# Kernel tuning notes

Hardware: AMD Instinct MI355X
Metric: run time of the kernel (lower is better)

Reference implementation:

```python
import jax, jax.numpy as jnp
import numpy as np

CAPACITY = 65536
HIDDEN = 512
NUM_HASHES = 8
HASH_SIZE = 16
BATCH = 2048


def setup_inputs() -> dict:
    key = jax.random.key(0)
    ks = jax.random.split(key, 6)
    scale = 1.0 / np.sqrt(HIDDEN)
    query = jax.random.normal(ks[0], (BATCH, HIDDEN), dtype=jnp.float32)
    memory_keys = jax.random.normal(ks[1], (CAPACITY, HIDDEN), dtype=jnp.float32) * scale
    memory_values = jax.random.normal(ks[2], (CAPACITY, HIDDEN), dtype=jnp.float32) * scale
    hash_projections = jax.random.normal(ks[3], (NUM_HASHES, HIDDEN, HASH_SIZE), dtype=jnp.float32) * scale
    out_w = jax.random.normal(ks[4], (HIDDEN, HIDDEN), dtype=jnp.float32) * scale  # torch Linear weight [out,in]
    out_b = jnp.zeros((HIDDEN,), dtype=jnp.float32)
    return {"query": query, "memory_keys": memory_keys, "memory_values": memory_values,
            "hash_projections": hash_projections, "out_w": out_w, "out_b": out_b, "top_k": 32}


def _compute_hash(x, hash_projections):
    # x: [m, h] -> hash bits [m, num_hashes] in {0,1}
    # einsum 'bh,nhd->bnd' then sum over d then sign-threshold
    proj = jnp.einsum('mh,nhd->mnd', x, hash_projections)
    return (proj.sum(-1) > 0).astype(jnp.int32)


def reference(query, memory_keys, memory_values, hash_projections, out_w, out_b, top_k):
    b, h = query.shape
    q_hash = _compute_hash(query, hash_projections)                    # [b, n]
    k_hash = _compute_hash(memory_keys, hash_projections)              # [c, n] (no_grad in torch)
    # Hamming distance via +/-1 dot product: dot = n - 2*dist (avoids [b,c,n] bool tensor)
    qf = (q_hash * 2 - 1).astype(jnp.float32)
    kf = (k_hash * 2 - 1).astype(jnp.float32)
    dot = jnp.einsum('bn,cn->bc', qf, kf)                              # [b, c]
    hash_dist = ((NUM_HASHES - dot) * 0.5).astype(jnp.int32)           # [b, c]
    k = min(top_k, memory_keys.shape[0])
    _, top_indices = jax.lax.top_k(-hash_dist, k)                      # smallest distances, [b, k]
    selected_keys = memory_keys[top_indices]                           # [b, k, h]
    selected_values = memory_values[top_indices]                       # [b, k, h]
    scores = jnp.einsum('bh,bkh->bk', query, selected_keys) / np.sqrt(h).astype(np.float32)
    attn = jax.nn.softmax(scores, axis=-1)
    memory_output = jnp.einsum('bk,bkh->bh', attn, selected_values)    # [b, h]
    return memory_output @ out_w.T + out_b
```

## Files before the change

kernel.cpp:

```cpp
#include <hip/hip_runtime.h>
#include <stdint.h>

#define BATCH  2048
#define HID    512
#define CAP    65536
#define NHASH  8
#define TOPK   32
#define NSLICE 16
#define SLICE_SZ (CAP / NSLICE)
#define ROWS_TILE 16

typedef unsigned int   u32;
typedef unsigned long long u64;
typedef double d4 __attribute__((ext_vector_type(4)));

__global__ __launch_bounds__(256) void k_psum(const float* __restrict__ proj,
                                              double* __restrict__ psumT) {
    int h = blockIdx.x * blockDim.x + threadIdx.x;
    if (h >= HID) return;
    for (int n = 0; n < NHASH; n++) {
        const float* p = proj + ((size_t)n * HID + h) * 16;
        double s = 0.0;
        #pragma unroll
        for (int d = 0; d < 16; d++) s += (double)p[d];
        psumT[(size_t)h * NHASH + n] = s;
    }
}

__global__ __launch_bounds__(256, 3) void k_hash(const float* __restrict__ x, int rows,
                                                 const double* __restrict__ psumT,
                                                 unsigned char* __restrict__ outb,
                                                 u32* __restrict__ hist16, int do_hist) {
    __shared__ __align__(16) float sX[ROWS_TILE * HID];
    __shared__ double sAcc4[4][ROWS_TILE][8];

    const int tid  = threadIdx.x;
    const int w    = tid >> 6;
    const int m    = (tid & 63) & 15;
    const int kk   = (tid & 63) >> 4;

    d4 z = {0.0, 0.0, 0.0, 0.0};
    d4 pr = __builtin_amdgcn_mfma_f64_16x16x4f64((double)(m + 1), 1.0, z, 0, 0, 0);
    d4 pc = __builtin_amdgcn_mfma_f64_16x16x4f64(1.0, (double)(m + 1), z, 0, 0, 0);
    d4 pp = __builtin_amdgcn_mfma_f64_16x16x4f64((double)(1 << kk),
                                                 (double)(1 << (4 * kk)), z, 0, 0, 0);
    int rowOf[4], colOf[4];
    #pragma unroll
    for (int i = 0; i < 4; i++) {
        rowOf[i] = (int)(pr[i] * 0.25) - 1;
        colOf[i] = (int)(pc[i] * 0.25) - 1;
    }
    u32 pb = (u32)pp[0];
    u32 pairPacked = 0;
    #pragma unroll
    for (int e = 0; e < 16; e++)
        if ((pb >> e) & 1u) pairPacked |= (u32)(e & 3) << (2 * (e >> 2));

    const int kAdj = (int)((pairPacked >> (2 * kk)) & 3u);
    double bfrag[32];
    #pragma unroll
    for (int j = 0; j < 32; j++) {
        int kp = 128 * w + 4 * j + kAdj;
        bfrag[j] = (m < 8) ? psumT[(size_t)kp * NHASH + m] : 0.0;
    }

    const int sw = (m & 7) << 2;
    const int nTiles = rows / ROWS_TILE;

    for (int t = blockIdx.x; t < nTiles; t += gridDim.x) {
        const int rowBase = t * ROWS_TILE;

        for (int i = tid; i < ROWS_TILE * 128; i += 256) {
            int r = i >> 7, G = i & 127;
            float4 v = ((const float4*)(x + (size_t)(rowBase + r) * HID))[G];
            ((float4*)sX)[r * 128 + (G ^ (r & 7))] = v;
        }
        __syncthreads();

        d4 acc = {0.0, 0.0, 0.0, 0.0};
        const float* sxm = sX + m * HID;
        #pragma unroll
        for (int j = 0; j < 32; j++) {
            int k = 128 * w + 4 * j + kk;
            double a = (double)sxm[k ^ sw];
            acc = __builtin_amdgcn_mfma_f64_16x16x4f64(a, bfrag[j], acc, 0, 0, 0);
        }
        #pragma unroll
        for (int i = 0; i < 4; i++) {
            if (((unsigned)rowOf[i] < (unsigned)ROWS_TILE) && ((unsigned)colOf[i] < 8u))
                sAcc4[w][rowOf[i]][colOf[i]] = acc[i];
        }
        __syncthreads();

        if (tid < ROWS_TILE) {
            u32 byte = 0;
            #pragma unroll
            for (int n = 0; n < 8; n++) {
                double s = sAcc4[0][tid][n] + sAcc4[1][tid][n]
                         + sAcc4[2][tid][n] + sAcc4[3][tid][n];
                if (s > 0.0) byte |= (1u << n);
            }
            outb[rowBase + tid] = (unsigned char)byte;
            if (do_hist) atomicAdd(&hist16[((rowBase + tid) / SLICE_SZ) * 256 + byte], 1u);
        }
    }
}

__global__ __launch_bounds__(256) void k_scan(const u32* __restrict__ hist16,
                                              u32* __restrict__ bucketCnt,
                                              u32* __restrict__ bucketOff,
                                              u32* __restrict__ off16) {
    __shared__ u32 sh[256], sh2[256];
    int v = threadIdx.x;
    u32 tot = 0;
    for (int s = 0; s < NSLICE; s++) tot += hist16[s * 256 + v];
    bucketCnt[v] = tot;
    sh[v] = tot;
    __syncthreads();
    if (v == 0) {
        u32 run = 0;
        for (int u = 0; u < 256; u++) { sh2[u] = run; run += sh[u]; }
    }
    __syncthreads();
    u32 base = sh2[v];
    bucketOff[v] = base;
    for (int s = 0; s < NSLICE; s++) { off16[s * 256 + v] = base; base += hist16[s * 256 + v]; }
}

__global__ __launch_bounds__(256) void k_compact(const unsigned char* __restrict__ khash,
                                                 const u32* __restrict__ off16,
                                                 u32* __restrict__ bucketList) {
    __shared__ unsigned char sh[SLICE_SZ];
    int s  = blockIdx.x & (NSLICE - 1);
    int bg = blockIdx.x >> 4;
    ((uint4*)sh)[threadIdx.x] = ((const uint4*)(khash + (size_t)s * SLICE_SZ))[threadIdx.x];
    __syncthreads();
    int w = threadIdx.x >> 6, lane = threadIdx.x & 63;
    int v = bg * 4 + w;
    u32 base = off16[s * 256 + v];
    for (int i = 0; i < SLICE_SZ / 64; i++) {
        int c = i * 64 + lane;
        unsigned char byte = sh[c];
        bool hit = (byte == (unsigned char)v);
        u64 m = __ballot(hit);
        if (hit) {
            int rank = __popcll(m & ((1ull << lane) - 1ull));
            bucketList[base + rank] = (u32)(s * SLICE_SZ + c);
        }
        base += (u32)__popcll(m);
    }
}

__global__ __launch_bounds__(256) void k_select(const unsigned char* __restrict__ qhash,
                                                const u32* __restrict__ bucketCnt,
                                                const u32* __restrict__ bucketOff,
                                                const u32* __restrict__ bucketList,
                                                int* __restrict__ topIdx) {
    __shared__ u32 sCnt[256], sOff[256];
    __shared__ int sPos[4];
    int tid = threadIdx.x;
    sCnt[tid] = bucketCnt[tid];
    sOff[tid] = bucketOff[tid];
    int w = tid >> 6, lane = tid & 63;
    if (lane == 0) sPos[w] = 0;
    __syncthreads();

    int q = blockIdx.x * 4 + w;
    u32 qh = qhash[q];

    int d[4]; u32 cnt[4], off[4];
    #pragma unroll
    for (int jj = 0; jj < 4; jj++) {
        int v = lane + jj * 64;
        d[jj] = __popc(qh ^ (u32)v);
        cnt[jj] = sCnt[v];
        off[jj] = sOff[v];
    }

    u32 ct[9];
    #pragma unroll
    for (int t = 0; t < 9; t++) {
        u32 c = 0;
        #pragma unroll
        for (int jj = 0; jj < 4; jj++) c += (d[jj] == t) ? cnt[jj] : 0u;
        #pragma unroll
        for (int s = 32; s >= 1; s >>= 1) c += __shfl_xor(c, s, 64);
        ct[t] = c;
    }

    int dcut = 0; u32 run = 0, before = 0;
    for (int t = 0; t < 9; t++) {
        before = run; run += ct[t];
        if (run >= TOPK) { dcut = t; break; }
    }
    int need = TOPK - (int)before;

    #pragma unroll
    for (int jj = 0; jj < 4; jj++) {
        if (d[jj] < dcut && cnt[jj] > 0) {
            int base = atomicAdd(&sPos[w], (int)cnt[jj]);
            for (u32 e = 0; e < cnt[jj]; e++)
                topIdx[q * TOPK + base + e] = (int)bucketList[off[jj] + e];
        }
    }

    int nb = 0;
    #pragma unroll
    for (int jj = 0; jj < 4; jj++) nb += (d[jj] == dcut) ? 1 : 0;
    #pragma unroll
    for (int s = 32; s >= 1; s >>= 1) nb += __shfl_xor(nb, s, 64);

    if (nb == 1) {
        u32 boff = 0xFFFFFFFFu;
        #pragma unroll
        for (int jj = 0; jj < 4; jj++) if (d[jj] == dcut) boff = off[jj];
        #pragma unroll
        for (int s = 32; s >= 1; s >>= 1) boff = min(boff, __shfl_xor(boff, s, 64));
        if (lane < need)
            topIdx[q * TOPK + (int)before + lane] = (int)bucketList[boff + lane];
    } else {
        u32 pos[4], end[4]; int val[4];
        #pragma unroll
        for (int jj = 0; jj < 4; jj++) {
            if (d[jj] == dcut && cnt[jj] > 0) {
                pos[jj] = off[jj]; end[jj] = off[jj] + cnt[jj];
                val[jj] = (int)bucketList[pos[jj]];
            } else { pos[jj] = 0; end[jj] = 0; val[jj] = 0x7fffffff; }
        }
        for (int it = 0; it < need; it++) {
            int m = min(min(val[0], val[1]), min(val[2], val[3]));
            int g = m;
            #pragma unroll
            for (int s = 32; s >= 1; s >>= 1) g = min(g, __shfl_xor(g, s, 64));
            if (lane == 0) topIdx[q * TOPK + (int)before + it] = g;
            if (m == g && g != 0x7fffffff) {
                #pragma unroll
                for (int jj = 0; jj < 4; jj++) {
                    if (val[jj] == g) {
                        pos[jj]++;
                        val[jj] = (pos[jj] < end[jj]) ? (int)bucketList[pos[jj]] : 0x7fffffff;
                        break;
                    }
                }
            }
        }
    }
}

__global__ __launch_bounds__(256) void k_attn(const float* __restrict__ keys,
                                              const float* __restrict__ vals,
                                              const float* __restrict__ query,
                                              const int* __restrict__ topIdx,
                                              float* __restrict__ mo) {
    __shared__ int sIdx[TOPK];
    __shared__ float sSc[TOPK], sE[TOPK];
    int b = blockIdx.x, tid = threadIdx.x;
    if (tid < TOPK) sIdx[tid] = topIdx[b * TOPK + tid];
    __syncthreads();

    int w = tid >> 6, lane = tid & 63;
    const float4* qp = (const float4*)(query + (size_t)b * HID + lane * 8);
    float4 qa = qp[0], qb = qp[1];

    for (int i = w * 8; i < w * 8 + 8; i++) {
        int idx = sIdx[i];
        const float4* kp = (const float4*)(keys + (size_t)idx * HID + lane * 8);
        float4 ka = kp[0], kb = kp[1];
        float dot = qa.x * ka.x + qa.y * ka.y + qa.z * ka.z + qa.w * ka.w
                  + qb.x * kb.x + qb.y * kb.y + qb.z * kb.z + qb.w * kb.w;
        #pragma unroll
        for (int s = 32; s >= 1; s >>= 1) dot += __shfl_xor(dot, s, 64);
        if (lane == 0) sSc[i] = dot * 0.04419417382415922f;
    }
    __syncthreads();

    if (tid < TOPK) {
        float m = -1e30f;
        for (int i = 0; i < TOPK; i++) m = fmaxf(m, sSc[i]);
        sE[tid] = expf(sSc[tid] - m);
    }
    __syncthreads();

    float sum = 0.f;
    for (int i = 0; i < TOPK; i++) sum += sE[i];
    float inv = 1.0f / sum;

    int h0 = tid, h1 = tid + 256;
    float a0 = 0.f, a1 = 0.f;
    for (int i = 0; i < TOPK; i++) {
        int idx = sIdx[i];
        float e = sE[i];
        a0 += e * vals[(size_t)idx * HID + h0];
        a1 += e * vals[(size_t)idx * HID + h1];
    }
    mo[(size_t)b * HID + h0] = a0 * inv;
    mo[(size_t)b * HID + h1] = a1 * inv;
}

__global__ __launch_bounds__(256) void k_transpose(const float* __restrict__ w,
                                                   float* __restrict__ wt) {
    __shared__ float tile[64][65];
    int bx = blockIdx.x, by = blockIdx.y;
    int tx = threadIdx.x & 63, ty = threadIdx.x >> 6;
    for (int r = ty; r < 64; r += 4)
        tile[r][tx] = w[(size_t)(by * 64 + r) * HID + bx * 64 + tx];
    __syncthreads();
    for (int r = ty; r < 64; r += 4)
        wt[(size_t)(bx * 64 + r) * HID + by * 64 + tx] = tile[tx][r];
}

__global__ __launch_bounds__(256) void k_proj(const float* __restrict__ mo,
                                              const float* __restrict__ wt,
                                              const float* __restrict__ bias,
                                              float* __restrict__ out) {
    int tid = threadIdx.x;
    int o = (blockIdx.x & 1) * 256 + tid;
    int bb = (blockIdx.x >> 1) * 8;
    float acc[8];
    #pragma unroll
    for (int r = 0; r < 8; r++) acc[r] = 0.f;
    for (int h = 0; h < HID; h++) {
        float wv = wt[(size_t)h * HID + o];
        #pragma unroll
        for (int r = 0; r < 8; r++)
            acc[r] += mo[(size_t)(bb + r) * HID + h] * wv;
    }
    float bv = bias[o];
    #pragma unroll
    for (int r = 0; r < 8; r++)
        out[(size_t)(bb + r) * HID + o] = acc[r] + bv;
}

extern "C" void kernel_launch(void* const* d_in, const int* in_sizes, int n_in,
                              void* d_out, int out_size, void* d_ws, size_t ws_size,
                              hipStream_t stream) {
    const float* query = (const float*)d_in[0];
    const float* keys  = (const float*)d_in[1];
    const float* vals  = (const float*)d_in[2];
    const float* proj  = (const float*)d_in[3];
    const float* outw  = (const float*)d_in[4];
    const float* outb  = (const float*)d_in[5];
    float* out = (float*)d_out;

    char* ws = (char*)d_ws;
    double*        psumT      = (double*)(ws + 0);
    unsigned char* qhash      = (unsigned char*)(ws + 32768);
    unsigned char* khash      = (unsigned char*)(ws + 34816);
    u32*           hist16     = (u32*)(ws + 100352);
    u32*           bucketCnt  = (u32*)(ws + 116736);
    u32*           bucketOff  = (u32*)(ws + 117760);
    u32*           off16      = (u32*)(ws + 118784);
    u32*           bucketList = (u32*)(ws + 135168);
    int*           topIdx     = (int*)(ws + 397312);
    float*         mo         = (float*)(ws + 659456);
    float*         wt         = (float*)(ws + 4853760);
    (void)in_sizes; (void)n_in; (void)out_size; (void)ws_size;

    hipMemsetAsync(hist16, 0, 16384, stream);
    k_psum<<<2, 256, 0, stream>>>(proj, psumT);
    k_hash<<<128, 256, 0, stream>>>(query, BATCH, psumT, qhash, hist16, 0);
    k_hash<<<1024, 256, 0, stream>>>(keys, CAP, psumT, khash, hist16, 1);
    k_scan<<<1, 256, 0, stream>>>(hist16, bucketCnt, bucketOff, off16);
    k_compact<<<1024, 256, 0, stream>>>(khash, off16, bucketList);
    k_select<<<BATCH / 4, 256, 0, stream>>>(qhash, bucketCnt, bucketOff, bucketList, topIdx);
    k_attn<<<BATCH, 256, 0, stream>>>(keys, vals, query, topIdx, mo);
    k_transpose<<<dim3(8, 8), 256, 0, stream>>>(outw, wt);
    k_proj<<<512, 256, 0, stream>>>(mo, wt, outb, out);
}
```

Measured before the change: 384.4 us.

## Fuse launches: merge prep kernels, query/key hashing, and selection into attention

Merges the memset, psum and weight transpose into one prep kernel, and runs query and key hashing in a single launch. Top-k selection now happens inside the attention kernel, where wave 0 writes the indices straight to shared memory, so the topIdx buffer and its round trip go away. The scan uses a wave-shuffle prefix instead of a serial loop, and the value accumulation uses float2 loads. The aim is to cut launch count and serial overhead. The cost is that the other waves in each attention block sit idle while wave 0 does the selection.

```diff
diff --git a/kernel.cpp b/kernel.cpp
--- a/kernel.cpp
+++ b/kernel.cpp
@@ -9,28 +9,50 @@
 #define NSLICE 16
 #define SLICE_SZ (CAP / NSLICE)
 #define ROWS_TILE 16
+#define QTILES (BATCH / ROWS_TILE)
+#define KTILES (CAP / ROWS_TILE)
+#define QGRID  128
+#define KGRID  1024
 
 typedef unsigned int   u32;
 typedef unsigned long long u64;
 typedef double d4 __attribute__((ext_vector_type(4)));
 
-__global__ __launch_bounds__(256) void k_psum(const float* __restrict__ proj,
-                                              double* __restrict__ psumT) {
-    int h = blockIdx.x * blockDim.x + threadIdx.x;
-    if (h >= HID) return;
-    for (int n = 0; n < NHASH; n++) {
-        const float* p = proj + ((size_t)n * HID + h) * 16;
-        double s = 0.0;
-        #pragma unroll
-        for (int d = 0; d < 16; d++) s += (double)p[d];
-        psumT[(size_t)h * NHASH + n] = s;
-    }
-}
-
-__global__ __launch_bounds__(256, 3) void k_hash(const float* __restrict__ x, int rows,
+__global__ __launch_bounds__(256) void k_prep(const float* __restrict__ proj,
+                                              double* __restrict__ psumT,
+                                              u32* __restrict__ hist16,
+                                              const float* __restrict__ w,
+                                              float* __restrict__ wt) {
+    __shared__ float tile[64][65];
+    int bi = blockIdx.x, tid = threadIdx.x;
+    if (bi < 2) {
+        int g = bi * 256 + tid;
+        for (int i = g; i < NSLICE * 256; i += 512) hist16[i] = 0;
+        int h = g;
+        for (int n = 0; n < NHASH; n++) {
+            const float* p = proj + ((size_t)n * HID + h) * 16;
+            double s = 0.0;
+            #pragma unroll
+            for (int d = 0; d < 16; d++) s += (double)p[d];
+            psumT[(size_t)h * NHASH + n] = s;
+        }
+    } else {
+        int b = bi - 2, bx = b & 7, by = b >> 3;
+        int tx = tid & 63, ty = tid >> 6;
+        for (int r = ty; r < 64; r += 4)
+            tile[r][tx] = w[(size_t)(by * 64 + r) * HID + bx * 64 + tx];
+        __syncthreads();
+        for (int r = ty; r < 64; r += 4)
+            wt[(size_t)(bx * 64 + r) * HID + by * 64 + tx] = tile[tx][r];
+    }
+}
+
+__global__ __launch_bounds__(256, 3) void k_hash(const float* __restrict__ query,
+                                                 const float* __restrict__ keys,
                                                  const double* __restrict__ psumT,
-                                                 unsigned char* __restrict__ outb,
-                                                 u32* __restrict__ hist16, int do_hist) {
+                                                 unsigned char* __restrict__ qhash,
+                                                 unsigned char* __restrict__ khash,
+                                                 u32* __restrict__ hist16) {
     __shared__ __align__(16) float sX[ROWS_TILE * HID];
     __shared__ double sAcc4[4][ROWS_TILE][8];
 
@@ -38,6 +60,14 @@
     const int w    = tid >> 6;
     const int m    = (tid & 63) & 15;
     const int kk   = (tid & 63) >> 4;
+
+    const int isQ = (blockIdx.x < QGRID);
+    const float* x        = isQ ? query : keys;
+    unsigned char* outb   = isQ ? qhash : khash;
+    const int nTiles      = isQ ? QTILES : KTILES;
+    const int b0          = isQ ? blockIdx.x : (blockIdx.x - QGRID);
+    const int gstride     = isQ ? QGRID : KGRID;
+    const int do_hist     = !isQ;
 
     d4 z = {0.0, 0.0, 0.0, 0.0};
     d4 pr = __builtin_amdgcn_mfma_f64_16x16x4f64((double)(m + 1), 1.0, z, 0, 0, 0);
@@ -65,9 +95,8 @@
     }
 
     const int sw = (m & 7) << 2;
-    const int nTiles = rows / ROWS_TILE;
-
-    for (int t = blockIdx.x; t < nTiles; t += gridDim.x) {
+
+    for (int t = b0; t < nTiles; t += gstride) {
         const int rowBase = t * ROWS_TILE;
 
         for (int i = tid; i < ROWS_TILE * 128; i += 256) {
@@ -110,19 +139,22 @@
                                               u32* __restrict__ bucketCnt,
                                               u32* __restrict__ bucketOff,
                                               u32* __restrict__ off16) {
-    __shared__ u32 sh[256], sh2[256];
-    int v = threadIdx.x;
+    __shared__ u32 wsum[4];
+    int v = threadIdx.x, lane = v & 63, wv = v >> 6;
     u32 tot = 0;
     for (int s = 0; s < NSLICE; s++) tot += hist16[s * 256 + v];
     bucketCnt[v] = tot;
-    sh[v] = tot;
-    __syncthreads();
-    if (v == 0) {
-        u32 run = 0;
-        for (int u = 0; u < 256; u++) { sh2[u] = run; run += sh[u]; }
-    }
-    __syncthreads();
-    u32 base = sh2[v];
+    u32 inc = tot;
+    #pragma unroll
+    for (int s = 1; s < 64; s <<= 1) {
+        u32 n = __shfl_up(inc, s, 64);
+        if (lane >= s) inc += n;
+    }
+    if (lane == 63) wsum[wv] = inc;
+    __syncthreads();
+    u32 wof = 0;
+    for (int i = 0; i < wv; i++) wof += wsum[i];
+    u32 base = wof + inc - tot;
     bucketOff[v] = base;
     for (int s = 0; s < NSLICE; s++) { off16[s * 256 + v] = base; base += hist16[s * 256 + v]; }
 }
@@ -151,114 +183,104 @@
     }
 }
 
-__global__ __launch_bounds__(256) void k_select(const unsigned char* __restrict__ qhash,
-                                                const u32* __restrict__ bucketCnt,
-                                                const u32* __restrict__ bucketOff,
-                                                const u32* __restrict__ bucketList,
-                                                int* __restrict__ topIdx) {
-    __shared__ u32 sCnt[256], sOff[256];
-    __shared__ int sPos[4];
-    int tid = threadIdx.x;
-    sCnt[tid] = bucketCnt[tid];
-    sOff[tid] = bucketOff[tid];
+__global__ __launch_bounds__(256) void k_attn(const float* __restrict__ keys,
+                                              const float* __restrict__ vals,
+                                              const float* __restrict__ query,
+                                              const unsigned char* __restrict__ qhash,
+                                              const u32* __restrict__ bucketCnt,
+                                              const u32* __restrict__ bucketOff,
+                                              const u32* __restrict__ bucketList,
+                                              float* __restrict__ mo) {
+    __shared__ int sIdx[TOPK];
+    __shared__ float sSc[TOPK], sE[TOPK];
+    __shared__ int sPos0;
+    int b = blockIdx.x, tid = threadIdx.x;
     int w = tid >> 6, lane = tid & 63;
-    if (lane == 0) sPos[w] = 0;
-    __syncthreads();
-
-    int q = blockIdx.x * 4 + w;
-    u32 qh = qhash[q];
-
-    int d[4]; u32 cnt[4], off[4];
-    #pragma unroll
-    for (int jj = 0; jj < 4; jj++) {
-        int v = lane + jj * 64;
-        d[jj] = __popc(qh ^ (u32)v);
-        cnt[jj] = sCnt[v];
-        off[jj] = sOff[v];
-    }
-
-    u32 ct[9];
-    #pragma unroll
-    for (int t = 0; t < 9; t++) {
-        u32 c = 0;
-        #pragma unroll
-        for (int jj = 0; jj < 4; jj++) c += (d[jj] == t) ? cnt[jj] : 0u;
-        #pragma unroll
-        for (int s = 32; s >= 1; s >>= 1) c += __shfl_xor(c, s, 64);
-        ct[t] = c;
-    }
-
-    int dcut = 0; u32 run = 0, before = 0;
-    for (int t = 0; t < 9; t++) {
-        before = run; run += ct[t];
-        if (run >= TOPK) { dcut = t; break; }
-    }
-    int need = TOPK - (int)before;
-
-    #pragma unroll
-    for (int jj = 0; jj < 4; jj++) {
-        if (d[jj] < dcut && cnt[jj] > 0) {
-            int base = atomicAdd(&sPos[w], (int)cnt[jj]);
-            for (u32 e = 0; e < cnt[jj]; e++)
-                topIdx[q * TOPK + base + e] = (int)bucketList[off[jj] + e];
-        }
-    }
-
-    int nb = 0;
-    #pragma unroll
-    for (int jj = 0; jj < 4; jj++) nb += (d[jj] == dcut) ? 1 : 0;
-    #pragma unroll
-    for (int s = 32; s >= 1; s >>= 1) nb += __shfl_xor(nb, s, 64);
-
-    if (nb == 1) {
-        u32 boff = 0xFFFFFFFFu;
-        #pragma unroll
-        for (int jj = 0; jj < 4; jj++) if (d[jj] == dcut) boff = off[jj];
-        #pragma unroll
-        for (int s = 32; s >= 1; s >>= 1) boff = min(boff, __shfl_xor(boff, s, 64));
-        if (lane < need)
-            topIdx[q * TOPK + (int)before + lane] = (int)bucketList[boff + lane];
-    } else {
-        u32 pos[4], end[4]; int val[4];
+
+    if (w == 0) {
+        if (lane == 0) sPos0 = 0;
+        u32 qh = qhash[b];
+
+        int d[4]; u32 cnt[4], off[4];
         #pragma unroll
         for (int jj = 0; jj < 4; jj++) {
-            if (d[jj] == dcut && cnt[jj] > 0) {
-                pos[jj] = off[jj]; end[jj] = off[jj] + cnt[jj];
-                val[jj] = (int)bucketList[pos[jj]];
-            } else { pos[jj] = 0; end[jj] = 0; val[jj] = 0x7fffffff; }
-        }
-        for (int it = 0; it < need; it++) {
-            int m = min(min(val[0], val[1]), min(val[2], val[3]));
-            int g = m;
-            #pragma unroll
-            for (int s = 32; s >= 1; s >>= 1) g = min(g, __shfl_xor(g, s, 64));
-            if (lane == 0) topIdx[q * TOPK + (int)before + it] = g;
-            if (m == g && g != 0x7fffffff) {
+            int v = lane + jj * 64;
+            d[jj] = __popc(qh ^ (u32)v);
+            cnt[jj] = bucketCnt[v];
+            off[jj] = bucketOff[v];
+        }
+
+        u32 ct[9];
+        #pragma unroll
+        for (int t = 0; t < 9; t++) {
+            u32 c = 0;
+            #pragma unroll
+            for (int jj = 0; jj < 4; jj++) c += (d[jj] == t) ? cnt[jj] : 0u;
+            #pragma unroll
+            for (int s = 32; s >= 1; s >>= 1) c += __shfl_xor(c, s, 64);
+            ct[t] = c;
+        }
+
+        int dcut = 0; u32 run = 0, before = 0;
+        for (int t = 0; t < 9; t++) {
+            before = run; run += ct[t];
+            if (run >= TOPK) { dcut = t; break; }
+        }
+        int need = TOPK - (int)before;
+
+        #pragma unroll
+        for (int jj = 0; jj < 4; jj++) {
+            if (d[jj] < dcut && cnt[jj] > 0) {
+                int base = atomicAdd(&sPos0, (int)cnt[jj]);
+                for (u32 e = 0; e < cnt[jj]; e++)
+                    sIdx[base + e] = (int)bucketList[off[jj] + e];
+            }
+        }
+
+        int nb = 0;
+        #pragma unroll
+        for (int jj = 0; jj < 4; jj++) nb += (d[jj] == dcut) ? 1 : 0;
+        #pragma unroll
+        for (int s = 32; s >= 1; s >>= 1) nb += __shfl_xor(nb, s, 64);
+
+        if (nb == 1) {
+            u32 boff = 0xFFFFFFFFu;
+            #pragma unroll
+            for (int jj = 0; jj < 4; jj++) if (d[jj] == dcut) boff = off[jj];
+            #pragma unroll
+            for (int s = 32; s >= 1; s >>= 1) boff = min(boff, __shfl_xor(boff, s, 64));
+            if (lane < need)
+                sIdx[(int)before + lane] = (int)bucketList[boff + lane];
+        } else {
+            u32 pos[4], end[4]; int val[4];
+            #pragma unroll
+            for (int jj = 0; jj < 4; jj++) {
+                if (d[jj] == dcut && cnt[jj] > 0) {
+                    pos[jj] = off[jj]; end[jj] = off[jj] + cnt[jj];
+                    val[jj] = (int)bucketList[pos[jj]];
+                } else { pos[jj] = 0; end[jj] = 0; val[jj] = 0x7fffffff; }
+            }
+            for (int it = 0; it < need; it++) {
+                int m = min(min(val[0], val[1]), min(val[2], val[3]));
+                int g = m;
                 #pragma unroll
-                for (int jj = 0; jj < 4; jj++) {
-                    if (val[jj] == g) {
-                        pos[jj]++;
-                        val[jj] = (pos[jj] < end[jj]) ? (int)bucketList[pos[jj]] : 0x7fffffff;
-                        break;
+                for (int s = 32; s >= 1; s >>= 1) g = min(g, __shfl_xor(g, s, 64));
+                if (lane == 0) sIdx[(int)before + it] = g;
+                if (m == g && g != 0x7fffffff) {
+                    #pragma unroll
+                    for (int jj = 0; jj < 4; jj++) {
+                        if (val[jj] == g) {
+                            pos[jj]++;
+                            val[jj] = (pos[jj] < end[jj]) ? (int)bucketList[pos[jj]] : 0x7fffffff;
+                            break;
+                        }
                     }
                 }
             }
         }
     }
-}
-
-__global__ __launch_bounds__(256) void k_attn(const float* __restrict__ keys,
-                                              const float* __restrict__ vals,
-                                              const float* __restrict__ query,
-                                              const int* __restrict__ topIdx,
-                                              float* __restrict__ mo) {
-    __shared__ int sIdx[TOPK];
-    __shared__ float sSc[TOPK], sE[TOPK];
-    int b = blockIdx.x, tid = threadIdx.x;
-    if (tid < TOPK) sIdx[tid] = topIdx[b * TOPK + tid];
-    __syncthreads();
-
-    int w = tid >> 6, lane = tid & 63;
+    __syncthreads();
+
     const float4* qp = (const float4*)(query + (size_t)b * HID + lane * 8);
     float4 qa = qp[0], qb = qp[1];
 
@@ -285,28 +307,15 @@
     for (int i = 0; i < TOPK; i++) sum += sE[i];
     float inv = 1.0f / sum;
 
-    int h0 = tid, h1 = tid + 256;
+    int h0 = tid * 2;
     float a0 = 0.f, a1 = 0.f;
     for (int i = 0; i < TOPK; i++) {
         int idx = sIdx[i];
         float e = sE[i];
-        a0 += e * vals[(size_t)idx * HID + h0];
-        a1 += e * vals[(size_t)idx * HID + h1];
-    }
-    mo[(size_t)b * HID + h0] = a0 * inv;
-    mo[(size_t)b * HID + h1] = a1 * inv;
-}
-
-__global__ __launch_bounds__(256) void k_transpose(const float* __restrict__ w,
-                                                   float* __restrict__ wt) {
-    __shared__ float tile[64][65];
-    int bx = blockIdx.x, by = blockIdx.y;
-    int tx = threadIdx.x & 63, ty = threadIdx.x >> 6;
-    for (int r = ty; r < 64; r += 4)
-        tile[r][tx] = w[(size_t)(by * 64 + r) * HID + bx * 64 + tx];
-    __syncthreads();
-    for (int r = ty; r < 64; r += 4)
-        wt[(size_t)(bx * 64 + r) * HID + by * 64 + tx] = tile[tx][r];
+        float2 vv = *(const float2*)(vals + (size_t)idx * HID + h0);
+        a0 += e * vv.x; a1 += e * vv.y;
+    }
+    ((float2*)(mo + (size_t)b * HID))[tid] = make_float2(a0 * inv, a1 * inv);
 }
 
 __global__ __launch_bounds__(256) void k_proj(const float* __restrict__ mo,
@@ -339,7 +348,7 @@
     const float* vals  = (const float*)d_in[2];
     const float* proj  = (const float*)d_in[3];
     const float* outw  = (const float*)d_in[4];
-    const float* outb  = (const float*)d_in[5];
+    const float* outbp = (const float*)d_in[5];
     float* out = (float*)d_out;
 
     char* ws = (char*)d_ws;
@@ -351,19 +360,14 @@
     u32*           bucketOff  = (u32*)(ws + 117760);
     u32*           off16      = (u32*)(ws + 118784);
     u32*           bucketList = (u32*)(ws + 135168);
-    int*           topIdx     = (int*)(ws + 397312);
-    float*         mo         = (float*)(ws + 659456);
-    float*         wt         = (float*)(ws + 4853760);
+    float*         mo         = (float*)(ws + 397312);
+    float*         wt         = (float*)(ws + 4591616);
     (void)in_sizes; (void)n_in; (void)out_size; (void)ws_size;
 
-    hipMemsetAsync(hist16, 0, 16384, stream);
-    k_psum<<<2, 256, 0, stream>>>(proj, psumT);
-    k_hash<<<128, 256, 0, stream>>>(query, BATCH, psumT, qhash, hist16, 0);
-    k_hash<<<1024, 256, 0, stream>>>(keys, CAP, psumT, khash, hist16, 1);
+    k_prep<<<66, 256, 0, stream>>>(proj, psumT, hist16, outw, wt);
+    k_hash<<<QGRID + KGRID, 256, 0, stream>>>(query, keys, psumT, qhash, khash, hist16);
     k_scan<<<1, 256, 0, stream>>>(hist16, bucketCnt, bucketOff, off16);
     k_compact<<<1024, 256, 0, stream>>>(khash, off16, bucketList);
-    k_select<<<BATCH / 4, 256, 0, stream>>>(qhash, bucketCnt, bucketOff, bucketList, topIdx);
-    k_attn<<<BATCH, 256, 0, stream>>>(keys, vals, query, topIdx, mo);
-    k_transpose<<<dim3(8, 8), 256, 0, stream>>>(outw, wt);
-    k_proj<<<512, 256, 0, stream>>>(mo, wt, outb, out);
-}
+    k_attn<<<BATCH, 256, 0, stream>>>(keys, vals, query, qhash, bucketCnt, bucketOff, bucketList, mo);
+    k_proj<<<512, 256, 0, stream>>>(mo, wt, outbp, out);
+}
```

Result: faster. 367.4 us (-4.4%).
